# Performance work log

Measured on AMD Instinct MI355X. Metric: run time of the kernel, lower is better.

Reference implementation:

```python
import jax, jax.numpy as jnp
import numpy as np

K = 20          # n_neighbors
EPS = 1e-5      # batchnorm eps
SLOPE = 0.2     # leaky relu slope (DGCNN default)


def _bn_lrelu(x, axes):
    # batch-norm (per-batch stats, gamma=1, beta=0) + LeakyReLU(0.2)
    m = jnp.mean(x, axis=axes, keepdims=True)
    v = jnp.var(x, axis=axes, keepdims=True)
    return jax.nn.leaky_relu((x - m) * jax.lax.rsqrt(v + EPS), SLOPE)


def _knn(x_cf, k):
    # x_cf: (B, C, N) -> idx (B, N, k) of k nearest neighbors (incl. self)
    inner = jnp.einsum('bcn,bcm->bnm', x_cf, x_cf)
    sq = jnp.sum(x_cf * x_cf, axis=1)                  # (B, N)
    neg_d = 2.0 * inner - sq[:, :, None] - sq[:, None, :]
    return jax.lax.top_k(neg_d, k)[1]


def _gather(x_nl, idx):
    # x_nl: (B, N, C), idx: (B, N, k) -> (B, N, k, C) neighbor features
    return jnp.take_along_axis(x_nl[:, :, None, :], idx[..., None], axis=1)


def setup_inputs() -> dict:
    key = jax.random.key(0)
    ks = jax.random.split(key, 11)
    B, N, C = 16, 2048, 3
    dims = [64, 64, 128, 256]
    feat_dim = 1024

    def w(k, o, i):
        return jax.random.normal(k, (o, i), jnp.float32) / np.sqrt(i)

    return {
        'x': jax.random.normal(ks[0], (B, N, C), jnp.float32),
        'w_edge': w(ks[1], dims[0], 2 * C),
        'b_edge': jnp.zeros((dims[0],), jnp.float32),
        'w1': w(ks[2], dims[1], dims[0]),
        'b1': jnp.zeros((dims[1],), jnp.float32),
        'w2': w(ks[3], dims[2], dims[1]),
        'b2': jnp.zeros((dims[2],), jnp.float32),
        'w3': w(ks[4], dims[3], dims[2]),
        'b3': jnp.zeros((dims[3],), jnp.float32),
        'w_final': w(ks[5], feat_dim, sum(dims)),
        'b_final': jnp.zeros((feat_dim,), jnp.float32),
    }


def reference(x, w_edge, b_edge, w1, b1, w2, b2, w3, b3, w_final, b_final):
    # x: (B, N, 3) point cloud
    x_cf = jnp.transpose(x, (0, 2, 1))                 # (B, 3, N)
    idx = _knn(x_cf, K)                                # (B, N, k) -- graph built once

    # get_graph_features: edge feature = concat(neighbor - center, center)
    nb = _gather(x, idx)                               # (B, N, k, 3)
    ctr = jnp.broadcast_to(x[:, :, None, :], nb.shape)
    feat = jnp.concatenate([nb - ctr, ctr], axis=-1)   # (B, N, k, 6)

    # EdgeConvLayer: 1x1 conv2d + BN + LeakyReLU, then max over neighbors
    h = jnp.einsum('oc,bnkc->bonk', w_edge, feat) + b_edge[None, :, None, None]
    h = _bn_lrelu(h, (0, 2, 3))
    h = jnp.max(h, axis=3)                             # (B, 64, N)

    xs = [h]
    for w, b in ((w1, b1), (w2, b2), (w3, b3)):
        # graph_max_pooling with reused kNN indices
        g = jnp.max(_gather(jnp.transpose(h, (0, 2, 1)), idx), axis=2)  # (B, N, C)
        h = jnp.einsum('oc,bnc->bon', w, g) + b[None, :, None]          # 1x1 conv1d
        h = _bn_lrelu(h, (0, 2))
        xs.append(h)

    h_cat = jnp.concatenate(xs, axis=1)                # (B, 512, N)
    out = jnp.einsum('oc,bcn->bon', w_final, h_cat) + b_final[None, :, None]
    return jnp.max(out, axis=2)                        # (B, 1024)
```

## Files before the change

kernel.cpp:

```cpp
#include <hip/hip_runtime.h>
#include <hip/hip_bf16.h>
#include <math.h>

#define B_ 16
#define N_ 2048
#define KNN 20
#define SLOPE 0.2f
#define EPS_ 1e-5f

#define SEG 8
#define SEGLEN (N_ / SEG)
#define QPB 64
#define CAP 64

typedef __attribute__((ext_vector_type(8))) short short8;
typedef __attribute__((ext_vector_type(4))) float float4v;

__global__ __launch_bounds__(256, 2) void knn_kernel(const float* __restrict__ x,
                                                     int* __restrict__ idx,
                                                     const float* __restrict__ w_edge,
                                                     const float* __restrict__ b_edge,
                                                     float* __restrict__ cat,
                                                     double* __restrict__ stats) {
    __shared__ float4 pts4[N_];
    __shared__ union {
        float thr[QPB * 24];
        int sidx[QPB * KNN];
    } u2;
    __shared__ float tq[QPB];
    __shared__ int cnt[QPB];
    __shared__ float lv[QPB * CAP];
    __shared__ unsigned short li[QPB * CAP];
    __shared__ float ws[64 * 6];
    __shared__ float bs[64];
    __shared__ float s_sum[64], s_sq[64];

    const int b = blockIdx.x >> 5;
    const int qb = blockIdx.x & 31;
    const float* xb = x + (size_t)b * N_ * 3;
    for (int i = threadIdx.x; i < N_; i += 256) {
        float xv = xb[i * 3], yv = xb[i * 3 + 1], zv = xb[i * 3 + 2];
        pts4[i] = make_float4(xv, yv, zv, xv * xv + yv * yv + zv * zv);
    }
    for (int i = threadIdx.x; i < 64 * 6; i += 256) ws[i] = w_edge[i];
    if (threadIdx.x < QPB) {
        cnt[threadIdx.x] = 0;
        bs[threadIdx.x] = b_edge[threadIdx.x];
        s_sum[threadIdx.x] = 0.f; s_sq[threadIdx.x] = 0.f;
    }
    __syncthreads();

    const int s = threadIdx.x >> 5;
    const int qs = threadIdx.x & 31;
    const int q0 = qs * 2, q1 = q0 + 1;
    const int n0 = qb * QPB + q0;
    const float4 pa = pts4[n0];
    const float4 pb = pts4[n0 + 1];
    const int m0 = s * SEGLEN;

    float ca[8], cb[8];
#pragma unroll
    for (int c = 0; c < 8; ++c) {
        float va0 = -INFINITY, va1 = -INFINITY;
        float vb0 = -INFINITY, vb1 = -INFINITY;
        for (int g = 0; g < 4; ++g) {
            float4 r[8];
#pragma unroll
            for (int j = 0; j < 8; ++j) r[j] = pts4[m0 + c * 32 + g * 8 + j];
#pragma unroll
            for (int j = 0; j < 8; ++j) {
                const float da = 2.f * (pa.x * r[j].x + pa.y * r[j].y + pa.z * r[j].z)
                                 - pa.w - r[j].w;
                const float db = 2.f * (pb.x * r[j].x + pb.y * r[j].y + pb.z * r[j].z)
                                 - pb.w - r[j].w;
                if (j & 1) { va1 = fmaxf(va1, da); vb1 = fmaxf(vb1, db); }
                else       { va0 = fmaxf(va0, da); vb0 = fmaxf(vb0, db); }
            }
        }
        ca[c] = fmaxf(va0, va1); cb[c] = fmaxf(vb0, vb1);
    }
    {
        float t0 = -INFINITY, t1 = -INFINITY, t2 = -INFINITY;
        float u0 = -INFINITY, u1 = -INFINITY, u2v = -INFINITY;
#pragma unroll
        for (int c = 0; c < 8; ++c) {
            float v = ca[c];
            float r0 = fminf(t0, v); t0 = fmaxf(t0, v);
            float r1 = fminf(t1, r0); t1 = fmaxf(t1, r0);
            t2 = fmaxf(t2, r1);
            float w = cb[c];
            float s0 = fminf(u0, w); u0 = fmaxf(u0, w);
            float s1 = fminf(u1, s0); u1 = fmaxf(u1, s0);
            u2v = fmaxf(u2v, s1);
        }
        u2.thr[q0 * 24 + s * 3 + 0] = t0;
        u2.thr[q0 * 24 + s * 3 + 1] = t1;
        u2.thr[q0 * 24 + s * 3 + 2] = t2;
        u2.thr[q1 * 24 + s * 3 + 0] = u0;
        u2.thr[q1 * 24 + s * 3 + 1] = u1;
        u2.thr[q1 * 24 + s * 3 + 2] = u2v;
    }
    __syncthreads();

    if (threadIdx.x < QPB) {
        const int qq = threadIdx.x;
        float s0 = INFINITY, s1 = INFINITY, s2 = INFINITY, s3 = INFINITY, s4 = INFINITY;
#pragma unroll
        for (int j = 0; j < 24; ++j) {
            float c = u2.thr[qq * 24 + j];
            float u;
            u = fminf(s0, c); c = fmaxf(s0, c); s0 = u;
            u = fminf(s1, c); c = fmaxf(s1, c); s1 = u;
            u = fminf(s2, c); c = fmaxf(s2, c); s2 = u;
            u = fminf(s3, c); c = fmaxf(s3, c); s3 = u;
            s4 = fminf(s4, c);
        }
        tq[qq] = s4 - (fabsf(s4) * 1e-6f + 1e-6f);
    }
    __syncthreads();

    const float ta = tq[q0];
    const float tb = tq[q1];
    for (int g = 0; g < 32; ++g) {
        float4 r[8];
#pragma unroll
        for (int j = 0; j < 8; ++j) r[j] = pts4[m0 + g * 8 + j];
#pragma unroll
        for (int j = 0; j < 8; ++j) {
            const int m = m0 + g * 8 + j;
            const float da = 2.f * (pa.x * r[j].x + pa.y * r[j].y + pa.z * r[j].z)
                             - pa.w - r[j].w;
            const float db = 2.f * (pb.x * r[j].x + pb.y * r[j].y + pb.z * r[j].z)
                             - pb.w - r[j].w;
            if (da >= ta) {
                int pos = atomicAdd(&cnt[q0], 1);
                if (pos < CAP) { lv[q0 * CAP + pos] = da; li[q0 * CAP + pos] = (unsigned short)m; }
            }
            if (db >= tb) {
                int pos = atomicAdd(&cnt[q1], 1);
                if (pos < CAP) { lv[q1 * CAP + pos] = db; li[q1 * CAP + pos] = (unsigned short)m; }
            }
        }
    }
    __syncthreads();

    if (threadIdx.x < QPB) {
        const int qq = threadIdx.x;
        const int nn = qb * QPB + qq;
        int* op = idx + (size_t)(b * N_ + nn) * KNN;
        float vals[KNN]; int inds[KNN];
#pragma unroll
        for (int j = 0; j < KNN; ++j) { vals[j] = -INFINITY; inds[j] = 0; }
        const int c = cnt[qq];
        if (c <= CAP) {
            for (int j = 0; j < c; ++j) {
                const float v = lv[qq * CAP + j];
                if (v > vals[KNN - 1]) {
                    float cv = v; int ci = li[qq * CAP + j];
#pragma unroll
                    for (int k = 0; k < KNN; ++k) {
                        const bool sw = cv > vals[k];
                        const float tv = vals[k]; const int ti = inds[k];
                        vals[k] = sw ? cv : tv;  inds[k] = sw ? ci : ti;
                        cv      = sw ? tv : cv;  ci      = sw ? ti : ci;
                    }
                }
            }
        } else {
            const float4 pq2 = pts4[nn];
            for (int m = 0; m < N_; ++m) {
                const float4 p = pts4[m];
                const float d = 2.f * (pq2.x * p.x + pq2.y * p.y + pq2.z * p.z)
                                - pq2.w - p.w;
                if (d > vals[KNN - 1]) {
                    float cv = d; int ci = m;
#pragma unroll
                    for (int k = 0; k < KNN; ++k) {
                        const bool sw = cv > vals[k];
                        const float tv = vals[k]; const int ti = inds[k];
                        vals[k] = sw ? cv : tv;  inds[k] = sw ? ci : ti;
                        cv      = sw ? tv : cv;  ci      = sw ? ti : ci;
                    }
                }
            }
        }
#pragma unroll
        for (int j = 0; j < KNN; ++j) {
            op[j] = inds[j];
            u2.sidx[qq * KNN + j] = inds[j];
        }
    }
    __syncthreads();

    {
        const int p = threadIdx.x >> 2;
        const int cg = threadIdx.x & 3;
        const int n = qb * QPB + p;
        const float4 ctr = pts4[n];
        const float cx = ctr.x, cy = ctr.y, cz = ctr.z;

        float co[16], maxv[16], sum[16], sq[16];
#pragma unroll
        for (int i = 0; i < 16; ++i) {
            const int o = cg * 16 + i;
            const float* wr = &ws[o * 6];
            co[i] = bs[o] + wr[3] * cx + wr[4] * cy + wr[5] * cz;
            maxv[i] = -INFINITY; sum[i] = 0.f; sq[i] = 0.f;
        }

        for (int k = 0; k < KNN; ++k) {
            const int j = u2.sidx[p * KNN + k];
            const float4 nb = pts4[j];
            const float dx = nb.x - cx, dy = nb.y - cy, dz = nb.z - cz;
#pragma unroll
            for (int i = 0; i < 16; ++i) {
                const float* wr = &ws[(cg * 16 + i) * 6];
                float h = co[i] + wr[0] * dx + wr[1] * dy + wr[2] * dz;
                sum[i] += h; sq[i] += h * h;
                maxv[i] = fmaxf(maxv[i], h);
            }
        }

        float* cp = cat + (size_t)(b * N_ + n) * 512 + cg * 16;
#pragma unroll
        for (int i4 = 0; i4 < 4; ++i4)
            *(float4*)&cp[i4 * 4] = make_float4(maxv[i4 * 4], maxv[i4 * 4 + 1],
                                                maxv[i4 * 4 + 2], maxv[i4 * 4 + 3]);
#pragma unroll
        for (int i = 0; i < 16; ++i) {
            atomicAdd(&s_sum[cg * 16 + i], sum[i]);
            atomicAdd(&s_sq[cg * 16 + i], sq[i]);
        }
    }
    __syncthreads();
    if (threadIdx.x < 64) {
        atomicAdd(&stats[threadIdx.x], (double)s_sum[threadIdx.x]);
        atomicAdd(&stats[64 + threadIdx.x], (double)s_sq[threadIdx.x]);
    }
}

__global__ __launch_bounds__(256) void wconv_kernel(const float* __restrict__ w,
                                                    __hip_bfloat16* __restrict__ wb) {
    int t = blockIdx.x * 256 + threadIdx.x;
    wb[t] = __float2bfloat16(w[t]);
}

template <int CIN, int COUT, int PT>
__global__ __launch_bounds__(256) void layer_kernel(float* __restrict__ cat,
                                                    const int* __restrict__ idx,
                                                    const float* __restrict__ w,
                                                    const float* __restrict__ bias,
                                                    const double* __restrict__ stats_in,
                                                    double invcnt_in,
                                                    double* __restrict__ stats_out,
                                                    int off_in, int off_out) {
    constexpr int P = 64;
    constexpr int LDC = CIN + 4;
    constexpr int WS = COUT + 4;
    constexpr int NCG = CIN / 4;
    constexpr int PPAR = 256 / NCG;
    constexpr int NOG = COUT / 4;
    static_assert(NOG * (P / PT) == 256, "thread mapping");

    __shared__ float g[P * LDC];
    __shared__ float wt[16 * WS];
    __shared__ float s_sum[COUT], s_sq[COUT];

    const int b = blockIdx.x & 15;
    const int pb = blockIdx.x >> 4;
    const int pt0 = b * N_ + pb * P;

    {
        const int cg = threadIdx.x % NCG;
        const int pp = threadIdx.x / NCG;
        float mean[4], inv[4];
#pragma unroll
        for (int j = 0; j < 4; ++j) {
            const double mu = stats_in[cg * 4 + j] * invcnt_in;
            const double e2 = stats_in[CIN + cg * 4 + j] * invcnt_in;
            const float var = (float)(e2 - mu * mu);
            mean[j] = (float)mu;
            inv[j] = rsqrtf(var + EPS_);
        }
        for (int p = pp; p < P; p += PPAR) {
            const int* ip = idx + (size_t)(pt0 + p) * KNN;
            float4 m = make_float4(-INFINITY, -INFINITY, -INFINITY, -INFINITY);
#pragma unroll
            for (int k = 0; k < KNN; ++k) {
                const int j = ip[k];
                const float4 v = *(const float4*)&cat[(size_t)(b * N_ + j) * 512 + off_in + cg * 4];
                m.x = fmaxf(m.x, v.x); m.y = fmaxf(m.y, v.y);
                m.z = fmaxf(m.z, v.z); m.w = fmaxf(m.w, v.w);
            }
            float4 r;
            r.x = (m.x - mean[0]) * inv[0]; r.x = r.x >= 0.f ? r.x : SLOPE * r.x;
            r.y = (m.y - mean[1]) * inv[1]; r.y = r.y >= 0.f ? r.y : SLOPE * r.y;
            r.z = (m.z - mean[2]) * inv[2]; r.z = r.z >= 0.f ? r.z : SLOPE * r.z;
            r.w = (m.w - mean[3]) * inv[3]; r.w = r.w >= 0.f ? r.w : SLOPE * r.w;
            *(float4*)&g[p * LDC + cg * 4] = r;
        }
    }
    if (threadIdx.x < COUT) { s_sum[threadIdx.x] = 0.f; s_sq[threadIdx.x] = 0.f; }

    const int og = threadIdx.x % NOG;
    const int pg = threadIdx.x / NOG;
    const int o0 = og * 4, p0 = pg * PT;

    float acc[4][PT];
#pragma unroll
    for (int i = 0; i < 4; ++i)
#pragma unroll
        for (int j = 0; j < PT; ++j) acc[i][j] = 0.f;

    for (int c0 = 0; c0 < CIN; c0 += 16) {
        __syncthreads();
        for (int i = threadIdx.x; i < COUT * 16; i += 256) {
            int o = i >> 4, cc = i & 15;
            wt[cc * WS + o] = w[(size_t)o * CIN + c0 + cc];
        }
        __syncthreads();
#pragma unroll
        for (int ccq = 0; ccq < 4; ++ccq) {
            const float4 w0 = *(const float4*)&wt[(ccq * 4 + 0) * WS + o0];
            const float4 w1 = *(const float4*)&wt[(ccq * 4 + 1) * WS + o0];
            const float4 w2 = *(const float4*)&wt[(ccq * 4 + 2) * WS + o0];
            const float4 w3 = *(const float4*)&wt[(ccq * 4 + 3) * WS + o0];
#pragma unroll
            for (int p = 0; p < PT; ++p) {
                const float4 gv = *(const float4*)&g[(p0 + p) * LDC + c0 + ccq * 4];
                acc[0][p] += w0.x * gv.x; acc[0][p] += w1.x * gv.y;
                acc[0][p] += w2.x * gv.z; acc[0][p] += w3.x * gv.w;
                acc[1][p] += w0.y * gv.x; acc[1][p] += w1.y * gv.y;
                acc[1][p] += w2.y * gv.z; acc[1][p] += w3.y * gv.w;
                acc[2][p] += w0.z * gv.x; acc[2][p] += w1.z * gv.y;
                acc[2][p] += w2.z * gv.z; acc[2][p] += w3.z * gv.w;
                acc[3][p] += w0.w * gv.x; acc[3][p] += w1.w * gv.y;
                acc[3][p] += w2.w * gv.z; acc[3][p] += w3.w * gv.w;
            }
        }
    }

    const float4 bv = *(const float4*)&bias[o0];
    float lsum[4] = {0.f, 0.f, 0.f, 0.f}, lsq[4] = {0.f, 0.f, 0.f, 0.f};
#pragma unroll
    for (int p = 0; p < PT; ++p) {
        float4 hv;
        hv.x = acc[0][p] + bv.x; hv.y = acc[1][p] + bv.y;
        hv.z = acc[2][p] + bv.z; hv.w = acc[3][p] + bv.w;
        lsum[0] += hv.x; lsq[0] += hv.x * hv.x;
        lsum[1] += hv.y; lsq[1] += hv.y * hv.y;
        lsum[2] += hv.z; lsq[2] += hv.z * hv.z;
        lsum[3] += hv.w; lsq[3] += hv.w * hv.w;
        *(float4*)&cat[(size_t)(pt0 + p0 + p) * 512 + off_out + o0] = hv;
    }
#pragma unroll
    for (int i = 0; i < 4; ++i) {
        atomicAdd(&s_sum[o0 + i], lsum[i]);
        atomicAdd(&s_sq[o0 + i], lsq[i]);
    }
    __syncthreads();
    if (threadIdx.x < COUT) {
        atomicAdd(&stats_out[threadIdx.x], (double)s_sum[threadIdx.x]);
        atomicAdd(&stats_out[COUT + threadIdx.x], (double)s_sq[threadIdx.x]);
    }
}

__global__ __launch_bounds__(256) void bnconv_kernel(const float* __restrict__ cat,
                                                     const double* __restrict__ stats,
                                                     unsigned short* __restrict__ catb,
                                                     double ik, double in_) {
    const int t = blockIdx.x * 256 + threadIdx.x;
    const int pn = t >> 7;
    const int c = (t & 127) * 4;

    const double* sp; const double* qp; double icnt;
    if (c < 64)       { sp = stats + c;             qp = stats + 64 + c;        icnt = ik; }
    else if (c < 128) { sp = stats + 128 + (c - 64);  qp = stats + 192 + (c - 64);  icnt = in_; }
    else if (c < 256) { sp = stats + 256 + (c - 128); qp = stats + 384 + (c - 128); icnt = in_; }
    else              { sp = stats + 512 + (c - 256); qp = stats + 768 + (c - 256); icnt = in_; }

    const float4 v = *(const float4*)&cat[(size_t)pn * 512 + c];
    float r[4]; const float vv[4] = {v.x, v.y, v.z, v.w};
#pragma unroll
    for (int j = 0; j < 4; ++j) {
        const double mu = sp[j] * icnt;
        const double e2 = qp[j] * icnt;
        const float var = (float)(e2 - mu * mu);
        const float inv = rsqrtf(var + EPS_);
        float x = (vv[j] - (float)mu) * inv;
        r[j] = x >= 0.f ? x : SLOPE * x;
    }
    ushort4 o;
    __hip_bfloat16 h0 = __float2bfloat16(r[0]); o.x = *(unsigned short*)&h0;
    __hip_bfloat16 h1 = __float2bfloat16(r[1]); o.y = *(unsigned short*)&h1;
    __hip_bfloat16 h2 = __float2bfloat16(r[2]); o.z = *(unsigned short*)&h2;
    __hip_bfloat16 h3 = __float2bfloat16(r[3]); o.w = *(unsigned short*)&h3;
    *(ushort4*)&catb[(size_t)pn * 512 + c] = o;
}

__global__ __launch_bounds__(256) void final_mfma_kernel(const short* __restrict__ catb,
                                                         const short* __restrict__ wb,
                                                         const float* __restrict__ bias,
                                                         float* __restrict__ partial) {
    constexpr int LDK = 72;
    __shared__ short As[128 * LDK];
    __shared__ short Bs[128 * LDK];
    __shared__ float red[256];

    const int bid = blockIdx.x;
    const int plo = bid & 7;
    const int ob = (bid >> 3) & 7;
    const int pblk = ((bid >> 6) << 3) | plo;
    const int pt0 = pblk * 128;

    const int wid = threadIdx.x >> 6;
    const int lane = threadIdx.x & 63;
    const int wm = wid >> 1, wn = wid & 1;
    const int lm = lane & 15, g = lane >> 4;

    const int srow = threadIdx.x >> 1;
    const int scg = (threadIdx.x & 1) * 32;
    const short* ga = catb + (size_t)(pt0 + srow) * 512 + scg;
    const short* gb = wb + (size_t)(ob * 128 + srow) * 512 + scg;
    short* la = As + srow * LDK + scg;
    short* lb = Bs + srow * LDK + scg;

    float4v acc[4][4];
#pragma unroll
    for (int i = 0; i < 4; ++i)
#pragma unroll
        for (int j = 0; j < 4; ++j) acc[i][j] = {0.f, 0.f, 0.f, 0.f};

    short8 ra[4], rb[4];
#pragma unroll
    for (int j = 0; j < 4; ++j) {
        ra[j] = *(const short8*)(ga + j * 8);
        rb[j] = *(const short8*)(gb + j * 8);
    }

    for (int step = 0; step < 8; ++step) {
        __syncthreads();
#pragma unroll
        for (int j = 0; j < 4; ++j) {
            *(short8*)(la + j * 8) = ra[j];
            *(short8*)(lb + j * 8) = rb[j];
        }
        __syncthreads();
        if (step < 7) {
            const int c1 = (step + 1) * 64;
#pragma unroll
            for (int j = 0; j < 4; ++j) {
                ra[j] = *(const short8*)(ga + c1 + j * 8);
                rb[j] = *(const short8*)(gb + c1 + j * 8);
            }
        }
#pragma unroll
        for (int kk = 0; kk < 2; ++kk) {
            short8 a[4], b[4];
#pragma unroll
            for (int t = 0; t < 4; ++t) {
                a[t] = *(const short8*)&As[(wm * 64 + t * 16 + lm) * LDK + kk * 32 + g * 8];
                b[t] = *(const short8*)&Bs[(wn * 64 + t * 16 + lm) * LDK + kk * 32 + g * 8];
            }
#pragma unroll
            for (int mt = 0; mt < 4; ++mt)
#pragma unroll
                for (int nt = 0; nt < 4; ++nt)
                    acc[mt][nt] = __builtin_amdgcn_mfma_f32_16x16x32_bf16(
                        a[mt], b[nt], acc[mt][nt], 0, 0, 0);
        }
    }

    float cm[4];
#pragma unroll
    for (int nt = 0; nt < 4; ++nt) {
        float m = -INFINITY;
#pragma unroll
        for (int mt = 0; mt < 4; ++mt)
#pragma unroll
            for (int r = 0; r < 4; ++r) m = fmaxf(m, acc[mt][nt][r]);
        m = fmaxf(m, __shfl_xor(m, 16, 64));
        m = fmaxf(m, __shfl_xor(m, 32, 64));
        cm[nt] = m;
    }
    __syncthreads();
    if (lane < 16) {
#pragma unroll
        for (int nt = 0; nt < 4; ++nt)
            red[wm * 128 + wn * 64 + nt * 16 + lane] = cm[nt];
    }
    __syncthreads();
    if (threadIdx.x < 128) {
        const int o = threadIdx.x;
        float v = fmaxf(red[o], red[128 + o]) + bias[ob * 128 + o];
        partial[(size_t)pblk * 1024 + ob * 128 + o] = v;
    }
}

__global__ __launch_bounds__(256) void reduce_kernel(const float* __restrict__ partial,
                                                     float* __restrict__ out) {
    int t = blockIdx.x * 256 + threadIdx.x;
    int b = t >> 10, o = t & 1023;
    float m = -INFINITY;
#pragma unroll 4
    for (int i = 0; i < 16; ++i)
        m = fmaxf(m, partial[(size_t)((b * 16 + i) * 1024) + o]);
    out[t] = m;
}

extern "C" void kernel_launch(void* const* d_in, const int* in_sizes, int n_in,
                              void* d_out, int out_size, void* d_ws, size_t ws_size,
                              hipStream_t stream) {
    const float* x = (const float*)d_in[0];
    const float* w_edge = (const float*)d_in[1];
    const float* b_edge = (const float*)d_in[2];
    const float* w1 = (const float*)d_in[3];
    const float* b1 = (const float*)d_in[4];
    const float* w2 = (const float*)d_in[5];
    const float* b2 = (const float*)d_in[6];
    const float* w3 = (const float*)d_in[7];
    const float* b3 = (const float*)d_in[8];
    const float* w_final = (const float*)d_in[9];
    const float* b_final = (const float*)d_in[10];
    float* out = (float*)d_out;

    char* ws = (char*)d_ws;
    int* idx = (int*)ws;
    float* cat = (float*)(ws + 2621440);
    float* partial = (float*)(ws + 69730304);
    double* stats = (double*)(ws + 70778880);
    __hip_bfloat16* catb = (__hip_bfloat16*)(ws + 70787072);
    __hip_bfloat16* wb = (__hip_bfloat16*)(ws + 104341504);

    double* st_e = stats;
    double* st_1 = stats + 128;
    double* st_2 = stats + 256;
    double* st_3 = stats + 512;
    const double ik = 1.0 / ((double)B_ * N_ * KNN);
    const double in_ = 1.0 / ((double)B_ * N_);

    hipMemsetAsync(stats, 0, 1024 * sizeof(double), stream);
    wconv_kernel<<<2048, 256, 0, stream>>>(w_final, wb);

    knn_kernel<<<B_ * 32, 256, 0, stream>>>(x, idx, w_edge, b_edge, cat, st_e);
    layer_kernel<64, 64, 4><<<(B_ * N_) / 64, 256, 0, stream>>>(
        cat, idx, w1, b1, st_e, ik, st_1, 0, 64);
    layer_kernel<64, 128, 8><<<(B_ * N_) / 64, 256, 0, stream>>>(
        cat, idx, w2, b2, st_1, in_, st_2, 64, 128);
    layer_kernel<128, 256, 16><<<(B_ * N_) / 64, 256, 0, stream>>>(
        cat, idx, w3, b3, st_2, in_, st_3, 128, 256);
    bnconv_kernel<<<(B_ * N_ * 128) / 256, 256, 0, stream>>>(
        cat, stats, (unsigned short*)catb, ik, in_);
    final_mfma_kernel<<<2048, 256, 0, stream>>>((const short*)catb, (const short*)wb,
                                                b_final, partial);
    reduce_kernel<<<64, 256, 0, stream>>>(partial, out);
}
```

Baseline: 354.2 us.

## Restructure kNN threshold pass: 16 segments, 4 queries per thread, rotated reads

The kNN kernel now splits candidates into 16 segments instead of 8, and each thread handles 4 query points instead of 2. This lets each loaded point be reused across more distance computations. The threshold now keeps the top-2 of 4 chunk maxima per segment, and the final threshold is the 13th-largest of 32 values rather than the 5th of 24. Each segment's reads are rotated by a segment-dependent offset to reduce LDS bank conflicts. The looser threshold may let more candidates into the per-query lists, raising the risk of overflowing CAP and falling back to the slow brute-force path.

```diff
diff --git a/kernel.cpp b/kernel.cpp
--- a/kernel.cpp
+++ b/kernel.cpp
@@ -8,7 +8,7 @@
 #define SLOPE 0.2f
 #define EPS_ 1e-5f
 
-#define SEG 8
+#define SEG 16
 #define SEGLEN (N_ / SEG)
 #define QPB 64
 #define CAP 64
@@ -24,7 +24,7 @@
                                                      double* __restrict__ stats) {
     __shared__ float4 pts4[N_];
     __shared__ union {
-        float thr[QPB * 24];
+        float thr[QPB * 32];
         int sidx[QPB * KNN];
     } u2;
     __shared__ float tq[QPB];
@@ -50,95 +50,109 @@
     }
     __syncthreads();
 
-    const int s = threadIdx.x >> 5;
-    const int qs = threadIdx.x & 31;
-    const int q0 = qs * 2, q1 = q0 + 1;
+    const int s = threadIdx.x >> 4;
+    const int qs = threadIdx.x & 15;
+    const int q0 = qs * 4;
     const int n0 = qb * QPB + q0;
-    const float4 pa = pts4[n0];
-    const float4 pb = pts4[n0 + 1];
+    const float4 pq0 = pts4[n0], pq1 = pts4[n0 + 1];
+    const float4 pq2 = pts4[n0 + 2], pq3 = pts4[n0 + 3];
     const int m0 = s * SEGLEN;
-
-    float ca[8], cb[8];
-#pragma unroll
-    for (int c = 0; c < 8; ++c) {
-        float va0 = -INFINITY, va1 = -INFINITY;
-        float vb0 = -INFINITY, vb1 = -INFINITY;
+    const int rot = s * 9;
+
+    float cm0[4], cm1[4], cm2[4], cm3[4];
+#pragma unroll
+    for (int c = 0; c < 4; ++c) {
+        float a0 = -INFINITY, a1 = -INFINITY;
+        float b0 = -INFINITY, b1 = -INFINITY;
+        float c0 = -INFINITY, c1 = -INFINITY;
+        float d0 = -INFINITY, d1 = -INFINITY;
         for (int g = 0; g < 4; ++g) {
             float4 r[8];
 #pragma unroll
-            for (int j = 0; j < 8; ++j) r[j] = pts4[m0 + c * 32 + g * 8 + j];
+            for (int j = 0; j < 8; ++j)
+                r[j] = pts4[m0 + ((c * 32 + g * 8 + j + rot) & (SEGLEN - 1))];
 #pragma unroll
             for (int j = 0; j < 8; ++j) {
-                const float da = 2.f * (pa.x * r[j].x + pa.y * r[j].y + pa.z * r[j].z)
-                                 - pa.w - r[j].w;
-                const float db = 2.f * (pb.x * r[j].x + pb.y * r[j].y + pb.z * r[j].z)
-                                 - pb.w - r[j].w;
-                if (j & 1) { va1 = fmaxf(va1, da); vb1 = fmaxf(vb1, db); }
-                else       { va0 = fmaxf(va0, da); vb0 = fmaxf(vb0, db); }
-            }
-        }
-        ca[c] = fmaxf(va0, va1); cb[c] = fmaxf(vb0, vb1);
+                const float da = 2.f * (pq0.x * r[j].x + pq0.y * r[j].y + pq0.z * r[j].z) - pq0.w - r[j].w;
+                const float db = 2.f * (pq1.x * r[j].x + pq1.y * r[j].y + pq1.z * r[j].z) - pq1.w - r[j].w;
+                const float dc = 2.f * (pq2.x * r[j].x + pq2.y * r[j].y + pq2.z * r[j].z) - pq2.w - r[j].w;
+                const float dd = 2.f * (pq3.x * r[j].x + pq3.y * r[j].y + pq3.z * r[j].z) - pq3.w - r[j].w;
+                if (j & 1) { a1 = fmaxf(a1, da); b1 = fmaxf(b1, db);
+                             c1 = fmaxf(c1, dc); d1 = fmaxf(d1, dd); }
+                else       { a0 = fmaxf(a0, da); b0 = fmaxf(b0, db);
+                             c0 = fmaxf(c0, dc); d0 = fmaxf(d0, dd); }
+            }
+        }
+        cm0[c] = fmaxf(a0, a1); cm1[c] = fmaxf(b0, b1);
+        cm2[c] = fmaxf(c0, c1); cm3[c] = fmaxf(d0, d1);
     }
     {
-        float t0 = -INFINITY, t1 = -INFINITY, t2 = -INFINITY;
-        float u0 = -INFINITY, u1 = -INFINITY, u2v = -INFINITY;
-#pragma unroll
-        for (int c = 0; c < 8; ++c) {
-            float v = ca[c];
-            float r0 = fminf(t0, v); t0 = fmaxf(t0, v);
-            float r1 = fminf(t1, r0); t1 = fmaxf(t1, r0);
-            t2 = fmaxf(t2, r1);
-            float w = cb[c];
-            float s0 = fminf(u0, w); u0 = fmaxf(u0, w);
-            float s1 = fminf(u1, s0); u1 = fmaxf(u1, s0);
-            u2v = fmaxf(u2v, s1);
-        }
-        u2.thr[q0 * 24 + s * 3 + 0] = t0;
-        u2.thr[q0 * 24 + s * 3 + 1] = t1;
-        u2.thr[q0 * 24 + s * 3 + 2] = t2;
-        u2.thr[q1 * 24 + s * 3 + 0] = u0;
-        u2.thr[q1 * 24 + s * 3 + 1] = u1;
-        u2.thr[q1 * 24 + s * 3 + 2] = u2v;
+#pragma unroll
+        for (int q = 0; q < 4; ++q) {
+            const float* cm = (q == 0) ? cm0 : (q == 1) ? cm1 : (q == 2) ? cm2 : cm3;
+            float t0 = -INFINITY, t1 = -INFINITY;
+#pragma unroll
+            for (int c = 0; c < 4; ++c) {
+                const float v = cm[c];
+                const float r0 = fminf(t0, v);
+                t0 = fmaxf(t0, v);
+                t1 = fmaxf(t1, r0);
+            }
+            u2.thr[(q0 + q) * 32 + s * 2 + 0] = t0;
+            u2.thr[(q0 + q) * 32 + s * 2 + 1] = t1;
+        }
     }
     __syncthreads();
 
     if (threadIdx.x < QPB) {
         const int qq = threadIdx.x;
-        float s0 = INFINITY, s1 = INFINITY, s2 = INFINITY, s3 = INFINITY, s4 = INFINITY;
-#pragma unroll
-        for (int j = 0; j < 24; ++j) {
-            float c = u2.thr[qq * 24 + j];
-            float u;
-            u = fminf(s0, c); c = fmaxf(s0, c); s0 = u;
-            u = fminf(s1, c); c = fmaxf(s1, c); s1 = u;
-            u = fminf(s2, c); c = fmaxf(s2, c); s2 = u;
-            u = fminf(s3, c); c = fmaxf(s3, c); s3 = u;
-            s4 = fminf(s4, c);
-        }
-        tq[qq] = s4 - (fabsf(s4) * 1e-6f + 1e-6f);
-    }
-    __syncthreads();
-
-    const float ta = tq[q0];
-    const float tb = tq[q1];
-    for (int g = 0; g < 32; ++g) {
+        float sm[13];
+#pragma unroll
+        for (int j = 0; j < 13; ++j) sm[j] = INFINITY;
+#pragma unroll
+        for (int j = 0; j < 32; ++j) {
+            float c = u2.thr[qq * 32 + j];
+#pragma unroll
+            for (int k = 0; k < 13; ++k) {
+                const float u = fminf(sm[k], c);
+                c = fmaxf(sm[k], c);
+                sm[k] = u;
+            }
+        }
+        tq[qq] = sm[12] - (fabsf(sm[12]) * 1e-6f + 1e-6f);
+    }
+    __syncthreads();
+
+    const float ta = tq[q0], tb = tq[q0 + 1], tc = tq[q0 + 2], td = tq[q0 + 3];
+    for (int g = 0; g < 16; ++g) {
         float4 r[8];
-#pragma unroll
-        for (int j = 0; j < 8; ++j) r[j] = pts4[m0 + g * 8 + j];
+        int mm[8];
 #pragma unroll
         for (int j = 0; j < 8; ++j) {
-            const int m = m0 + g * 8 + j;
-            const float da = 2.f * (pa.x * r[j].x + pa.y * r[j].y + pa.z * r[j].z)
-                             - pa.w - r[j].w;
-            const float db = 2.f * (pb.x * r[j].x + pb.y * r[j].y + pb.z * r[j].z)
-                             - pb.w - r[j].w;
+            mm[j] = m0 + ((g * 8 + j + rot) & (SEGLEN - 1));
+            r[j] = pts4[mm[j]];
+        }
+#pragma unroll
+        for (int j = 0; j < 8; ++j) {
+            const float da = 2.f * (pq0.x * r[j].x + pq0.y * r[j].y + pq0.z * r[j].z) - pq0.w - r[j].w;
+            const float db = 2.f * (pq1.x * r[j].x + pq1.y * r[j].y + pq1.z * r[j].z) - pq1.w - r[j].w;
+            const float dc = 2.f * (pq2.x * r[j].x + pq2.y * r[j].y + pq2.z * r[j].z) - pq2.w - r[j].w;
+            const float dd = 2.f * (pq3.x * r[j].x + pq3.y * r[j].y + pq3.z * r[j].z) - pq3.w - r[j].w;
             if (da >= ta) {
                 int pos = atomicAdd(&cnt[q0], 1);
-                if (pos < CAP) { lv[q0 * CAP + pos] = da; li[q0 * CAP + pos] = (unsigned short)m; }
+                if (pos < CAP) { lv[q0 * CAP + pos] = da; li[q0 * CAP + pos] = (unsigned short)mm[j]; }
             }
             if (db >= tb) {
-                int pos = atomicAdd(&cnt[q1], 1);
-                if (pos < CAP) { lv[q1 * CAP + pos] = db; li[q1 * CAP + pos] = (unsigned short)m; }
+                int pos = atomicAdd(&cnt[q0 + 1], 1);
+                if (pos < CAP) { lv[(q0 + 1) * CAP + pos] = db; li[(q0 + 1) * CAP + pos] = (unsigned short)mm[j]; }
+            }
+            if (dc >= tc) {
+                int pos = atomicAdd(&cnt[q0 + 2], 1);
+                if (pos < CAP) { lv[(q0 + 2) * CAP + pos] = dc; li[(q0 + 2) * CAP + pos] = (unsigned short)mm[j]; }
+            }
+            if (dd >= td) {
+                int pos = atomicAdd(&cnt[q0 + 3], 1);
+                if (pos < CAP) { lv[(q0 + 3) * CAP + pos] = dd; li[(q0 + 3) * CAP + pos] = (unsigned short)mm[j]; }
             }
         }
     }
@@ -167,11 +181,11 @@
                 }
             }
         } else {
-            const float4 pq2 = pts4[nn];
+            const float4 pqf = pts4[nn];
             for (int m = 0; m < N_; ++m) {
                 const float4 p = pts4[m];
-                const float d = 2.f * (pq2.x * p.x + pq2.y * p.y + pq2.z * p.z)
-                                - pq2.w - p.w;
+                const float d = 2.f * (pqf.x * p.x + pqf.y * p.y + pqf.z * p.z)
+                                - pqf.w - p.w;
                 if (d > vals[KNN - 1]) {
                     float cv = d; int ci = m;
 #pragma unroll
```

Result: no change. 356.9 us (+0.8%).
